# Performance work log

Measured on AMD Instinct MI355X. Metric: run time of the kernel, lower is better.

The kernel has to match this reference:

```python
import jax, jax.numpy as jnp
import numpy as np

B, T, E, H = 2, 2048, 1024, 16
HS = E // H  # head size 64


def setup_inputs() -> dict:
    key = jax.random.key(0)
    ks = jax.random.split(key, 6)
    s = 0.02
    return {
        "x": jax.random.normal(ks[0], (B, T, E), dtype=jnp.float32),
        "Wq": jax.random.normal(ks[1], (E, E), dtype=jnp.float32) * s,
        "Wk": jax.random.normal(ks[2], (E, E), dtype=jnp.float32) * s,
        "Wv": jax.random.normal(ks[3], (E, E), dtype=jnp.float32) * s,
        "Wp": jax.random.normal(ks[4], (E, E), dtype=jnp.float32) * s,
        "bp": jax.random.normal(ks[5], (E,), dtype=jnp.float32) * s,
    }


def reference(x, Wq, Wk, Wv, Wp, bp):
    b, t, e = x.shape
    # per-head projections (concatenated heads == single E->E matmul, reshaped)
    def heads(w):
        return jnp.einsum('bte,ef->btf', x, w).reshape(b, t, H, HS).transpose(0, 2, 1, 3)
    q, k, v = heads(Wq), heads(Wk), heads(Wv)  # [B,H,T,HS]
    # NOTE: original scales by full embed dim E, not head_size
    scores = jnp.einsum('bhqd,bhkd->bhqk', q, k) * (e ** -0.5)
    causal = jnp.tril(jnp.ones((t, t), dtype=bool))
    scores = jnp.where(causal, scores, -jnp.inf)
    probs = jax.nn.softmax(scores, axis=-1)
    # dropout is identity in eval mode
    out = jnp.einsum('bhqk,bhkd->bhqd', probs, v)  # [B,H,T,HS]
    out = out.transpose(0, 2, 1, 3).reshape(b, t, e)
    return jnp.einsum('bte,ef->btf', out, Wp) + bp
```

## Files before the change

### kernel.cpp

```cpp
#include <hip/hip_runtime.h>
#include <math.h>

typedef __bf16 bf16x8 __attribute__((ext_vector_type(8)));
typedef __bf16 bf16x4 __attribute__((ext_vector_type(4)));
typedef float f32x4 __attribute__((ext_vector_type(4)));

constexpr int Bb = 2, Tt = 2048, Ee = 1024, Hh = 16, Hs = 64;
constexpr int Mm = Bb * Tt;

__device__ inline unsigned short f2bf(float f) {
    union { float f; unsigned u; } c; c.f = f;
    unsigned u = c.u;
    u += 0x7FFFu + ((u >> 16) & 1u);
    return (unsigned short)(u >> 16);
}

#if __has_builtin(__builtin_amdgcn_exp2f)
#define EXP2(x) __builtin_amdgcn_exp2f(x)
#else
#define EXP2(x) exp2f(x)
#endif

__device__ inline void gl2lds16(const void* g, void* l) {
    __builtin_amdgcn_global_load_lds(
        (const __attribute__((address_space(1))) void*)g,
        (__attribute__((address_space(3))) void*)l, 16, 0, 0);
}

__device__ inline unsigned pk_bf16(float a, float b) {
    union { float f; unsigned u; } ca, cb;
    ca.f = a; cb.f = b;
    return __builtin_amdgcn_perm(ca.u + 0x8000u, cb.u + 0x8000u, 0x07060302u);
}

__device__ inline int gswz(int r) { return (r ^ (r >> 2)) & 3; }

__global__ __launch_bounds__(256) void prep(const float* __restrict__ x,
                                            const float* __restrict__ Wq,
                                            const float* __restrict__ Wk,
                                            const float* __restrict__ Wv,
                                            const float* __restrict__ Wp,
                                            unsigned short* __restrict__ xb,
                                            unsigned short* __restrict__ wt3,
                                            unsigned short* __restrict__ wpt) {
    const int tid = threadIdx.x;
    if (blockIdx.z == 4) {
        int flat = (blockIdx.y * 16 + blockIdx.x) * 256 + tid;
#pragma unroll
        for (int i = 0; i < 16; i++) {
            int gid = flat + i * 65536;
            float4 v = ((const float4*)x)[gid];
            ushort4 o;
            o.x = f2bf(v.x); o.y = f2bf(v.y); o.z = f2bf(v.z); o.w = f2bf(v.w);
            ((ushort4*)xb)[gid] = o;
        }
        return;
    }
    __shared__ unsigned short t[64][68];
    const float* W = (blockIdx.z == 0) ? Wq : (blockIdx.z == 1) ? Wk
                    : (blockIdx.z == 2) ? Wv : Wp;
    unsigned short* dst = (blockIdx.z < 3) ? wt3 + (size_t)blockIdx.z * 1024 * 1024 : wpt;
    const int k0 = blockIdx.x * 64, n0 = blockIdx.y * 64;
#pragma unroll
    for (int j = 0; j < 4; j++) {
        int row = (tid >> 4) + j * 16;
        int c4 = (tid & 15) * 4;
        float4 v = *(const float4*)&W[(size_t)(k0 + row) * 1024 + n0 + c4];
        t[row][c4 + 0] = f2bf(v.x); t[row][c4 + 1] = f2bf(v.y);
        t[row][c4 + 2] = f2bf(v.z); t[row][c4 + 3] = f2bf(v.w);
    }
    __syncthreads();
#pragma unroll
    for (int j = 0; j < 16; j++) {
        int flat = j * 256 + tid;
        int orow = flat >> 6, ocol = flat & 63;
        dst[(size_t)(n0 + orow) * 1024 + k0 + ocol] = t[ocol][orow];
    }
}

__device__ inline void gemm_mainloop(const unsigned short* __restrict__ A,
                                     const unsigned short* __restrict__ Bt,
                                     unsigned short* As, unsigned short* Bs,
                                     int bm, int bn, int tid, f32x4 (&acc)[4][4]) {
    const int lane = tid & 63, w = tid >> 6;
    const int quad = lane >> 4, cl = lane & 15;
    const int wm = (w >> 1) * 64, wn = (w & 1) * 64;

    auto stage = [&](int k0) {
#pragma unroll
        for (int i = 0; i < 2; i++) {
            int L = tid + i * 256;
            int r = L >> 2;
            int kc = (L & 3) ^ gswz(r);
            gl2lds16(A + (size_t)(bm + r) * 1024 + k0 + kc * 8, &As[L * 8]);
        }
#pragma unroll
        for (int i = 0; i < 2; i++) {
            int L = tid + i * 256;
            int r = L >> 2;
            int kc = (L & 3) ^ gswz(r);
            gl2lds16(Bt + (size_t)(bn + r) * 1024 + k0 + kc * 8, &Bs[L * 8]);
        }
    };

    stage(0);
    __syncthreads();
    for (int k0 = 0;;) {
        bf16x8 af[4], bfr[4];
#pragma unroll
        for (int mt = 0; mt < 4; mt++) {
            int r = wm + mt * 16 + cl;
            af[mt] = *(const bf16x8*)&As[(r * 4 + (quad ^ gswz(r))) * 8];
            int rb = wn + mt * 16 + cl;
            bfr[mt] = *(const bf16x8*)&Bs[(rb * 4 + (quad ^ gswz(rb))) * 8];
        }
#pragma unroll
        for (int mt = 0; mt < 4; mt++)
#pragma unroll
            for (int nt = 0; nt < 4; nt++)
                acc[mt][nt] = __builtin_amdgcn_mfma_f32_16x16x32_bf16(
                    af[mt], bfr[nt], acc[mt][nt], 0, 0, 0);
        k0 += 32;
        if (k0 >= 1024) break;
        __syncthreads();
        stage(k0);
        __syncthreads();
    }
}

__global__ __launch_bounds__(256, 2) void gemm_qkv(const unsigned short* __restrict__ A,
                                                   const unsigned short* __restrict__ Bt,
                                                   unsigned short* __restrict__ qb,
                                                   unsigned short* __restrict__ kb,
                                                   unsigned short* __restrict__ vtb) {
    __shared__ unsigned short As[128 * 32];
    __shared__ unsigned short Bs[128 * 32];
    const int tid = threadIdx.x;
    const int bm = blockIdx.y * 128;
    const int bn = blockIdx.x * 128;
    f32x4 acc[4][4] = {};
    gemm_mainloop(A, Bt, As, Bs, bm, bn, tid, acc);

    const int lane = tid & 63, w = tid >> 6;
    const int quad = lane >> 4, cl = lane & 15;
    const int wm = (w >> 1) * 64, wn = (w & 1) * 64;
    const int region = bn >> 10;

    if (region < 2) {
        unsigned short* dst = region ? kb : qb;
        const float qs = region ? 1.0f : 0.045084220027780107f;
#pragma unroll
        for (int mt = 0; mt < 4; mt++)
#pragma unroll
            for (int nt = 0; nt < 4; nt++)
#pragma unroll
                for (int rg = 0; rg < 4; rg++) {
                    int m = bm + wm + mt * 16 + quad * 4 + rg;
                    int nn = (bn + wn + nt * 16 + cl) & 1023;
                    int b = m >> 11, t = m & 2047, h = nn >> 6, hs = nn & 63;
                    dst[((size_t)(b * 16 + h) * 2048 + t) * 64 + hs] =
                        f2bf(acc[mt][nt][rg] * qs);
                }
    } else {
#pragma unroll
        for (int mt = 0; mt < 4; mt++) {
            int m0 = bm + wm + mt * 16 + quad * 4;
            int b = m0 >> 11, t0 = m0 & 2047;
#pragma unroll
            for (int nt = 0; nt < 4; nt++) {
                int nn = (bn + wn + nt * 16 + cl) & 1023;
                int h = nn >> 6, hs = nn & 63;
                ushort4 pk;
                pk.x = f2bf(acc[mt][nt][0]); pk.y = f2bf(acc[mt][nt][1]);
                pk.z = f2bf(acc[mt][nt][2]); pk.w = f2bf(acc[mt][nt][3]);
                *(ushort4*)&vtb[((size_t)(b * 16 + h) * 64 + hs) * 2048 + t0] = pk;
            }
        }
    }
}

__global__ __launch_bounds__(256, 4) void gemm_out(const unsigned short* __restrict__ A,
                                                   const unsigned short* __restrict__ Bt,
                                                   const float* __restrict__ bias,
                                                   float* __restrict__ out) {
    __shared__ unsigned short As[64 * 32];
    __shared__ unsigned short Bs[128 * 32];
    const int tid = threadIdx.x;
    const int bm = blockIdx.y * 64;
    const int bn = blockIdx.x * 128;
    const int lane = tid & 63, w = tid >> 6;
    const int quad = lane >> 4, cl = lane & 15;
    const int wm = (w >> 1) * 32, wn = (w & 1) * 64;
    f32x4 acc[2][4] = {};

    auto stage = [&](int k0) {
        {
            int L = tid;
            int r = L >> 2;
            int kc = (L & 3) ^ gswz(r);
            gl2lds16(A + (size_t)(bm + r) * 1024 + k0 + kc * 8, &As[L * 8]);
        }
#pragma unroll
        for (int i = 0; i < 2; i++) {
            int L = tid + i * 256;
            int r = L >> 2;
            int kc = (L & 3) ^ gswz(r);
            gl2lds16(Bt + (size_t)(bn + r) * 1024 + k0 + kc * 8, &Bs[L * 8]);
        }
    };

    stage(0);
    __syncthreads();
    for (int k0 = 0;;) {
        bf16x8 af[2], bfr[4];
#pragma unroll
        for (int mt = 0; mt < 2; mt++) {
            int r = wm + mt * 16 + cl;
            af[mt] = *(const bf16x8*)&As[(r * 4 + (quad ^ gswz(r))) * 8];
        }
#pragma unroll
        for (int nt = 0; nt < 4; nt++) {
            int rb = wn + nt * 16 + cl;
            bfr[nt] = *(const bf16x8*)&Bs[(rb * 4 + (quad ^ gswz(rb))) * 8];
        }
#pragma unroll
        for (int mt = 0; mt < 2; mt++)
#pragma unroll
            for (int nt = 0; nt < 4; nt++)
                acc[mt][nt] = __builtin_amdgcn_mfma_f32_16x16x32_bf16(
                    af[mt], bfr[nt], acc[mt][nt], 0, 0, 0);
        k0 += 32;
        if (k0 >= 1024) break;
        __syncthreads();
        stage(k0);
        __syncthreads();
    }

#pragma unroll
    for (int mt = 0; mt < 2; mt++)
#pragma unroll
        for (int nt = 0; nt < 4; nt++)
#pragma unroll
            for (int rg = 0; rg < 4; rg++) {
                int m = bm + wm + mt * 16 + quad * 4 + rg;
                int n = bn + wn + nt * 16 + cl;
                out[(size_t)m * 1024 + n] = acc[mt][nt][rg] + bias[n];
            }
}

__global__ __launch_bounds__(512, 2) void attn_mfma(const unsigned short* __restrict__ qg,
                                                    const unsigned short* __restrict__ kg,
                                                    const unsigned short* __restrict__ vtg,
                                                    unsigned short* __restrict__ og) {
    __shared__ unsigned short lds[32768];

    const int tid = threadIdx.x;
    const int idx = blockIdx.x;
    const int bh = idx & 31;
    const int j = idx >> 5;
    const int lane = tid & 63, w = tid >> 6;
    const int quad = lane >> 4, cl = lane & 15;
    const int g = w >> 2;
    const int qt = g ? (31 - j) : j;
    const int p = (w >> 1) & 1;
    const int qhalf = w & 1;
    const int qbase = qt * 64;
    const int qtL = 31 - j;
    const unsigned short* qB = qg + (size_t)bh * 2048 * 64;
    const unsigned short* kB = kg + (size_t)bh * 2048 * 64;
    const unsigned short* vB = vtg + (size_t)bh * 64 * 2048;

    float* Cmb = (float*)lds + g * 4608;
    float* Ll = Cmb + 4352;

    auto stageKV = [&](int kt) {
        unsigned short* Kd = lds + (kt & 3) * 4096;
        unsigned short* Vd = lds + 16384 + (kt & 3) * 4096;
        int L = tid;
        int r = L >> 3;
        int kc = (L & 7) ^ (r & 7);
        int grow = (r & 32) | ((r & 12) << 1) | ((r & 16) >> 2) | (r & 3);
        gl2lds16(kB + (size_t)(kt * 64 + grow) * 64 + kc * 8, &Kd[L * 8]);
        gl2lds16(vB + (size_t)r * 2048 + kt * 64 + kc * 8, &Vd[L * 8]);
    };

    bf16x8 qf[2][2];
#pragma unroll
    for (int nt2 = 0; nt2 < 2; nt2++)
#pragma unroll
        for (int kf = 0; kf < 2; kf++) {
            int row = qbase + qhalf * 32 + nt2 * 16 + cl;
            qf[nt2][kf] = *(const bf16x8*)&qB[(size_t)row * 64 + (kf * 4 + quad) * 8];
        }

    bf16x8 ones;
#pragma unroll
    for (int i = 0; i < 8; i++) ones[i] = (__bf16)1.0f;

    f32x4 oacc[2][4] = {};
    f32x4 lacc[2] = {};
    const int nit = (qtL + 2) >> 1;

    stageKV(0);
    stageKV(1);
    __syncthreads();

    for (int i = 0; i < nit; i++) {
        if (2 * i + 2 <= qtL) stageKV(2 * i + 2);
        if (2 * i + 3 <= qtL) stageKV(2 * i + 3);

        const int kt = 2 * i + p;
        if (kt <= qt) {
            const bool diag = (kt == qt);
            const unsigned short* Kl = lds + (kt & 3) * 4096;
            const unsigned short* Vl = lds + 16384 + (kt & 3) * 4096;
            f32x4 sac[4][2] = {};
            __builtin_amdgcn_s_setprio(1);
#pragma unroll
            for (int kf = 0; kf < 2; kf++)
#pragma unroll
                for (int mt = 0; mt < 4; mt++) {
                    int r = mt * 16 + cl, cc = kf * 4 + quad;
                    bf16x8 kf8 = *(const bf16x8*)&Kl[(r * 8 + (cc ^ (r & 7))) * 8];
#pragma unroll
                    for (int nt2 = 0; nt2 < 2; nt2++)
                        sac[mt][nt2] = __builtin_amdgcn_mfma_f32_16x16x32_bf16(
                            kf8, qf[nt2][kf], sac[mt][nt2], 0, 0, 0);
                }
            __builtin_amdgcn_s_setprio(0);
#pragma unroll
            for (int ks = 0; ks < 2; ks++) {
                bf16x8 pf[2];
#pragma unroll
                for (int nt2 = 0; nt2 < 2; nt2++) {
                    unsigned dw[4];
#pragma unroll
                    for (int mtl = 0; mtl < 2; mtl++) {
                        float pv[4];
#pragma unroll
                        for (int rg = 0; rg < 4; rg++) {
                            float e = EXP2(sac[ks * 2 + mtl][nt2][rg]);
                            if (diag && (ks * 32 + quad * 8 + mtl * 4 + rg >
                                         nt2 * 16 + cl + qhalf * 32))
                                e = 0.0f;
                            pv[rg] = e;
                        }
                        dw[mtl * 2 + 0] = pk_bf16(pv[1], pv[0]);
                        dw[mtl * 2 + 1] = pk_bf16(pv[3], pv[2]);
                    }
                    union { uint4 u; bf16x8 v; } cv;
                    cv.u = make_uint4(dw[0], dw[1], dw[2], dw[3]);
                    pf[nt2] = cv.v;
                }
                __builtin_amdgcn_s_setprio(1);
#pragma unroll
                for (int mt2 = 0; mt2 < 2; mt2++)
                    lacc[mt2] = __builtin_amdgcn_mfma_f32_16x16x32_bf16(
                        pf[mt2], ones, lacc[mt2], 0, 0, 0);
#pragma unroll
                for (int nt = 0; nt < 4; nt++) {
                    int r = nt * 16 + cl, cc = ks * 4 + quad;
                    bf16x8 vf = *(const bf16x8*)&Vl[(r * 8 + (cc ^ (r & 7))) * 8];
#pragma unroll
                    for (int mt2 = 0; mt2 < 2; mt2++)
                        oacc[mt2][nt] = __builtin_amdgcn_mfma_f32_16x16x32_bf16(
                            pf[mt2], vf, oacc[mt2][nt], 0, 0, 0);
                }
                __builtin_amdgcn_s_setprio(0);
            }
        }
        __syncthreads();
    }

    if (p == 1) {
#pragma unroll
        for (int mt2 = 0; mt2 < 2; mt2++)
#pragma unroll
            for (int rg = 0; rg < 4; rg++) {
                int row = qhalf * 32 + mt2 * 16 + quad * 4 + rg;
                if (cl == 0) Ll[row] = lacc[mt2][rg];
#pragma unroll
                for (int nt = 0; nt < 4; nt++)
                    Cmb[row * 68 + nt * 16 + cl] = oacc[mt2][nt][rg];
            }
    }
    __syncthreads();
    if (p == 0) {
        const int b = bh >> 4, h = bh & 15;
#pragma unroll
        for (int mt2 = 0; mt2 < 2; mt2++)
#pragma unroll
            for (int rg = 0; rg < 4; rg++) {
                int row = qhalf * 32 + mt2 * 16 + quad * 4 + rg;
                float inv = 1.0f / (lacc[mt2][rg] + Ll[row]);
                int t = qbase + row;
#pragma unroll
                for (int nt = 0; nt < 4; nt++) {
                    int hs = nt * 16 + cl;
                    float val = oacc[mt2][nt][rg] + Cmb[row * 68 + nt * 16 + cl];
                    og[((size_t)(b * 2048 + t)) * 1024 + h * 64 + hs] = f2bf(val * inv);
                }
            }
    }
}

extern "C" void kernel_launch(void* const* d_in, const int* in_sizes, int n_in,
                              void* d_out, int out_size, void* d_ws, size_t ws_size,
                              hipStream_t stream) {
    const float* x = (const float*)d_in[0];
    const float* Wq = (const float*)d_in[1];
    const float* Wk = (const float*)d_in[2];
    const float* Wv = (const float*)d_in[3];
    const float* Wp = (const float*)d_in[4];
    const float* bp = (const float*)d_in[5];
    float* out = (float*)d_out;

    unsigned short* xb = (unsigned short*)d_ws;
    unsigned short* wt3 = xb + (size_t)Mm * Ee;
    unsigned short* wpt = wt3 + (size_t)3 * Ee * Ee;
    unsigned short* qb = wpt + (size_t)Ee * Ee;
    unsigned short* kb = qb + (size_t)Mm * Ee;
    unsigned short* vtb = kb + (size_t)Mm * Ee;
    unsigned short* ab = vtb + (size_t)Mm * Ee;

    prep<<<dim3(16, 16, 5), dim3(256), 0, stream>>>(x, Wq, Wk, Wv, Wp, xb, wt3, wpt);
    gemm_qkv<<<dim3(24, 32), dim3(256), 0, stream>>>(xb, wt3, qb, kb, vtb);
    attn_mfma<<<dim3(512), dim3(512), 0, stream>>>(qb, kb, vtb, ab);
    gemm_out<<<dim3(8, 64), dim3(256), 0, stream>>>(ab, wpt, bp, out);
}
```

Before: 163.3 us.

## Rewrite QKV GEMM with 256x192 tiles and double-buffered ping-pong pipeline

Replaces the 128x128 single-buffered QKV GEMM mainloop with a 512-thread, 256x192 tile kernel using K=64 steps, double-buffered LDS, an 8-chunk XOR swizzle, and a hand-scheduled interleave of LDS reads, async global-to-LDS loads and MFMA bursts separated by barriers and explicit waitcnts with setprio. The aim is to overlap global loads with compute and raise arithmetic intensity per tile, cutting the per-iteration double syncthreads stalls. The grid shrinks to 256 blocks at one block per CU, which risks underfilling the 256-CU device and depends on the hand-tuned vmcnt counts being correct.

```diff
diff --git a/kernel.cpp b/kernel.cpp
--- a/kernel.cpp
+++ b/kernel.cpp
@@ -34,6 +34,10 @@
 }
 
 __device__ inline int gswz(int r) { return (r ^ (r >> 2)) & 3; }
+
+#define S_BARRIER() __builtin_amdgcn_s_barrier()
+#define WAIT_LGKM0() asm volatile("s_waitcnt lgkmcnt(0)" ::: "memory")
+#define WAIT_VM(n) asm volatile("s_waitcnt vmcnt(" #n ")" ::: "memory")
 
 __global__ __launch_bounds__(256) void prep(const float* __restrict__ x,
                                             const float* __restrict__ Wq,
@@ -78,102 +82,150 @@
     }
 }
 
-__device__ inline void gemm_mainloop(const unsigned short* __restrict__ A,
-                                     const unsigned short* __restrict__ Bt,
-                                     unsigned short* As, unsigned short* Bs,
-                                     int bm, int bn, int tid, f32x4 (&acc)[4][4]) {
-    const int lane = tid & 63, w = tid >> 6;
-    const int quad = lane >> 4, cl = lane & 15;
-    const int wm = (w >> 1) * 64, wn = (w & 1) * 64;
-
-    auto stage = [&](int k0) {
-#pragma unroll
-        for (int i = 0; i < 2; i++) {
-            int L = tid + i * 256;
-            int r = L >> 2;
-            int kc = (L & 3) ^ gswz(r);
-            gl2lds16(A + (size_t)(bm + r) * 1024 + k0 + kc * 8, &As[L * 8]);
-        }
-#pragma unroll
-        for (int i = 0; i < 2; i++) {
-            int L = tid + i * 256;
-            int r = L >> 2;
-            int kc = (L & 3) ^ gswz(r);
-            gl2lds16(Bt + (size_t)(bn + r) * 1024 + k0 + kc * 8, &Bs[L * 8]);
-        }
-    };
-
-    stage(0);
-    __syncthreads();
-    for (int k0 = 0;;) {
-        bf16x8 af[4], bfr[4];
-#pragma unroll
-        for (int mt = 0; mt < 4; mt++) {
-            int r = wm + mt * 16 + cl;
-            af[mt] = *(const bf16x8*)&As[(r * 4 + (quad ^ gswz(r))) * 8];
-            int rb = wn + mt * 16 + cl;
-            bfr[mt] = *(const bf16x8*)&Bs[(rb * 4 + (quad ^ gswz(rb))) * 8];
-        }
-#pragma unroll
-        for (int mt = 0; mt < 4; mt++)
-#pragma unroll
-            for (int nt = 0; nt < 4; nt++)
-                acc[mt][nt] = __builtin_amdgcn_mfma_f32_16x16x32_bf16(
-                    af[mt], bfr[nt], acc[mt][nt], 0, 0, 0);
-        k0 += 32;
-        if (k0 >= 1024) break;
-        __syncthreads();
-        stage(k0);
-        __syncthreads();
-    }
-}
-
-__global__ __launch_bounds__(256, 2) void gemm_qkv(const unsigned short* __restrict__ A,
+__global__ __launch_bounds__(512, 1) void gemm_qkv(const unsigned short* __restrict__ A,
                                                    const unsigned short* __restrict__ Bt,
                                                    unsigned short* __restrict__ qb,
                                                    unsigned short* __restrict__ kb,
                                                    unsigned short* __restrict__ vtb) {
-    __shared__ unsigned short As[128 * 32];
-    __shared__ unsigned short Bs[128 * 32];
+    __shared__ unsigned short As[2][16384];
+    __shared__ unsigned short Bs[2][12288];
     const int tid = threadIdx.x;
-    const int bm = blockIdx.y * 128;
-    const int bn = blockIdx.x * 128;
-    f32x4 acc[4][4] = {};
-    gemm_mainloop(A, Bt, As, Bs, bm, bn, tid, acc);
-
+    const int bm = blockIdx.y * 256;
+    const int bn = blockIdx.x * 192;
     const int lane = tid & 63, w = tid >> 6;
     const int quad = lane >> 4, cl = lane & 15;
-    const int wm = (w >> 1) * 64, wn = (w & 1) * 64;
-    const int region = bn >> 10;
-
-    if (region < 2) {
-        unsigned short* dst = region ? kb : qb;
-        const float qs = region ? 1.0f : 0.045084220027780107f;
-#pragma unroll
-        for (int mt = 0; mt < 4; mt++)
-#pragma unroll
-            for (int nt = 0; nt < 4; nt++)
+    const int wm = (w >> 1) * 64;
+    const int wn = (w & 1) * 96;
+
+    f32x4 acc[4][6] = {};
+    bf16x8 a[2][2];
+    bf16x8 b[6][2];
+
+    const int sr = tid >> 3, ss = tid & 7;
+    const int sc = ss ^ (sr & 7);
+
+    auto stA = [&](int buf, int u, int kt) {
+        gl2lds16(A + (size_t)(bm + u * 64 + sr) * 1024 + kt * 64 + sc * 8,
+                 &As[buf][u * 4096 + tid * 8]);
+    };
+    auto stB = [&](int buf, int u, int kt) {
+        gl2lds16(Bt + (size_t)(bn + u * 64 + sr) * 1024 + kt * 64 + sc * 8,
+                 &Bs[buf][u * 4096 + tid * 8]);
+    };
+    auto ldA = [&](int buf, int mh) {
+#pragma unroll
+        for (int mt = 0; mt < 2; mt++) {
+            int R = wm + mh * 32 + mt * 16 + cl;
+#pragma unroll
+            for (int kf = 0; kf < 2; kf++) {
+                int cc = kf * 4 + quad;
+                a[mt][kf] = *(const bf16x8*)&As[buf][(R * 8 + (cc ^ (R & 7))) * 8];
+            }
+        }
+    };
+    auto ldB = [&](int buf, int nh) {
+#pragma unroll
+        for (int nt = 0; nt < 3; nt++) {
+            int R = wn + nh * 48 + nt * 16 + cl;
+#pragma unroll
+            for (int kf = 0; kf < 2; kf++) {
+                int cc = kf * 4 + quad;
+                b[nh * 3 + nt][kf] = *(const bf16x8*)&Bs[buf][(R * 8 + (cc ^ (R & 7))) * 8];
+            }
+        }
+    };
+    auto mm = [&](int mh, int nh) {
+        __builtin_amdgcn_s_setprio(1);
+#pragma unroll
+        for (int mt = 0; mt < 2; mt++)
+#pragma unroll
+            for (int nt = 0; nt < 3; nt++)
+#pragma unroll
+                for (int kf = 0; kf < 2; kf++)
+                    acc[mh * 2 + mt][nh * 3 + nt] =
+                        __builtin_amdgcn_mfma_f32_16x16x32_bf16(
+                            a[mt][kf], b[nh * 3 + nt][kf],
+                            acc[mh * 2 + mt][nh * 3 + nt], 0, 0, 0);
+        __builtin_amdgcn_s_setprio(0);
+    };
+
+    stB(0, 0, 0); stB(0, 1, 0); stB(0, 2, 0);
+    stA(0, 0, 0); stA(0, 1, 0); stA(0, 2, 0); stA(0, 3, 0);
+    stB(1, 0, 1); stB(1, 1, 1); stB(1, 2, 1);
+    stA(1, 0, 1); stA(1, 1, 1); stA(1, 2, 1);
+    WAIT_VM(6);
+    S_BARRIER();
+
+    for (int j = 0; j < 8; ++j) {
+        const int ktc = 2 * j + 2, ktd = 2 * j + 3;
+        const bool pf = (j < 7);
+        ldA(0, 0); ldB(0, 0);
+        stA(1, 3, 2 * j + 1);
+        S_BARRIER(); WAIT_LGKM0();
+        mm(0, 0);
+        S_BARRIER();
+        ldB(0, 1);
+        S_BARRIER(); WAIT_LGKM0();
+        mm(0, 1);
+        S_BARRIER();
+        ldA(0, 1);
+        if (pf) { stB(0, 0, ktc); stB(0, 1, ktc); stB(0, 2, ktc); }
+        S_BARRIER(); WAIT_LGKM0();
+        mm(1, 1);
+        S_BARRIER();
+        if (pf) { stA(0, 0, ktc); stA(0, 1, ktc); stA(0, 2, ktc); }
+        if (pf) { WAIT_VM(6); } else { WAIT_VM(0); }
+        S_BARRIER();
+        mm(1, 0);
+        S_BARRIER();
+        ldA(1, 0); ldB(1, 0);
+        if (pf) stA(0, 3, ktc);
+        S_BARRIER(); WAIT_LGKM0();
+        mm(0, 0);
+        S_BARRIER();
+        ldB(1, 1);
+        S_BARRIER(); WAIT_LGKM0();
+        mm(0, 1);
+        S_BARRIER();
+        ldA(1, 1);
+        if (pf) { stB(1, 0, ktd); stB(1, 1, ktd); stB(1, 2, ktd); }
+        S_BARRIER(); WAIT_LGKM0();
+        mm(1, 1);
+        S_BARRIER();
+        if (pf) { stA(1, 0, ktd); stA(1, 1, ktd); stA(1, 2, ktd); }
+        if (pf) { WAIT_VM(6); } else { WAIT_VM(0); }
+        S_BARRIER();
+        mm(1, 0);
+        S_BARRIER();
+    }
+
+#pragma unroll
+    for (int ni = 0; ni < 6; ni++) {
+        int ncol = bn + wn + ni * 16 + cl;
+        int region = (bn + wn + ni * 16) >> 10;
+        int nn = ncol & 1023;
+        int h = nn >> 6, hs = nn & 63;
+        if (region < 2) {
+            unsigned short* dst = region ? kb : qb;
+            const float qs = region ? 1.0f : 0.045084220027780107f;
+#pragma unroll
+            for (int mi = 0; mi < 4; mi++)
 #pragma unroll
                 for (int rg = 0; rg < 4; rg++) {
-                    int m = bm + wm + mt * 16 + quad * 4 + rg;
-                    int nn = (bn + wn + nt * 16 + cl) & 1023;
-                    int b = m >> 11, t = m & 2047, h = nn >> 6, hs = nn & 63;
-                    dst[((size_t)(b * 16 + h) * 2048 + t) * 64 + hs] =
-                        f2bf(acc[mt][nt][rg] * qs);
+                    int m = bm + wm + mi * 16 + quad * 4 + rg;
+                    int b2 = m >> 11, t = m & 2047;
+                    dst[((size_t)(b2 * 16 + h) * 2048 + t) * 64 + hs] =
+                        f2bf(acc[mi][ni][rg] * qs);
                 }
-    } else {
-#pragma unroll
-        for (int mt = 0; mt < 4; mt++) {
-            int m0 = bm + wm + mt * 16 + quad * 4;
-            int b = m0 >> 11, t0 = m0 & 2047;
-#pragma unroll
-            for (int nt = 0; nt < 4; nt++) {
-                int nn = (bn + wn + nt * 16 + cl) & 1023;
-                int h = nn >> 6, hs = nn & 63;
+        } else {
+#pragma unroll
+            for (int mi = 0; mi < 4; mi++) {
+                int m0 = bm + wm + mi * 16 + quad * 4;
+                int b2 = m0 >> 11, t0 = m0 & 2047;
                 ushort4 pk;
-                pk.x = f2bf(acc[mt][nt][0]); pk.y = f2bf(acc[mt][nt][1]);
-                pk.z = f2bf(acc[mt][nt][2]); pk.w = f2bf(acc[mt][nt][3]);
-                *(ushort4*)&vtb[((size_t)(b * 16 + h) * 64 + hs) * 2048 + t0] = pk;
+                pk.x = f2bf(acc[mi][ni][0]); pk.y = f2bf(acc[mi][ni][1]);
+                pk.z = f2bf(acc[mi][ni][2]); pk.w = f2bf(acc[mi][ni][3]);
+                *(ushort4*)&vtb[((size_t)(b2 * 16 + h) * 64 + hs) * 2048 + t0] = pk;
             }
         }
     }
@@ -424,7 +476,7 @@
     unsigned short* ab = vtb + (size_t)Mm * Ee;
 
     prep<<<dim3(16, 16, 5), dim3(256), 0, stream>>>(x, Wq, Wk, Wv, Wp, xb, wt3, wpt);
-    gemm_qkv<<<dim3(24, 32), dim3(256), 0, stream>>>(xb, wt3, qb, kb, vtb);
+    gemm_qkv<<<dim3(16, 16), dim3(512), 0, stream>>>(xb, wt3, qb, kb, vtb);
     attn_mfma<<<dim3(512), dim3(512), 0, stream>>>(qb, kb, vtb, ab);
     gemm_out<<<dim3(8, 64), dim3(256), 0, stream>>>(ab, wpt, bp, out);
 }
```

Result: no change. 163.3 us (+0.0%).
